# Kernel tuning notes

Measured on AMD Instinct MI355X. Metric: run time of the kernel, lower is better.

Reference implementation:

```python
import jax, jax.numpy as jnp
import numpy as np
import math

B, S, HID = 1, 2048, 4096
NH, NKV, HD = 32, 8, 128
N_REP = NH // NKV
ROPE_THETA = 10000.0


def setup_inputs() -> dict:
    key = jax.random.key(0)
    ks = jax.random.split(key, 5)
    hidden_states = jax.random.normal(ks[0], (B, S, HID), dtype=jnp.float32)
    # additive causal mask: 0 on/below diagonal, -1e9 above
    causal = jnp.triu(jnp.full((S, S), -1e9, dtype=jnp.float32), k=1)
    attention_mask = causal[None, None, :, :]
    wq = jax.random.normal(ks[1], (HID, NH * HD), dtype=jnp.float32) * 0.02
    wk = jax.random.normal(ks[2], (HID, NKV * HD), dtype=jnp.float32) * 0.02
    wv = jax.random.normal(ks[3], (HID, NKV * HD), dtype=jnp.float32) * 0.02
    wo = jax.random.normal(ks[4], (NH * HD, HID), dtype=jnp.float32) * 0.02
    return {"hidden_states": hidden_states, "attention_mask": attention_mask,
            "wq": wq, "wk": wk, "wv": wv, "wo": wo}


def _rope_cos_sin(seq_len, head_dim, base, dtype):
    inv_freq = 1.0 / (base ** (jnp.arange(0, head_dim, 2, dtype=jnp.float32) / head_dim))
    t = jnp.arange(seq_len, dtype=jnp.float32)
    freqs = jnp.outer(t, inv_freq)          # [S, HD/2]
    emb = jnp.concatenate([freqs, freqs], axis=-1)  # [S, HD]
    return jnp.cos(emb).astype(dtype), jnp.sin(emb).astype(dtype)


def _rotate_interleaved(x):
    # pairs (x0,x1) -> (-x1, x0), interleaved (matches torch stack/reshape trick)
    xp = x.reshape(*x.shape[:-1], -1, 2)
    return jnp.stack([-xp[..., 1], xp[..., 0]], axis=-1).reshape(x.shape)


def reference(hidden_states, attention_mask, wq, wk, wv, wo):
    b, s, _ = hidden_states.shape
    q = (hidden_states @ wq).reshape(b, s, NH, HD).transpose(0, 2, 1, 3)   # [B,NH,S,HD]
    k = (hidden_states @ wk).reshape(b, s, NKV, HD).transpose(0, 2, 1, 3)  # [B,NKV,S,HD]
    v = (hidden_states @ wv).reshape(b, s, NKV, HD).transpose(0, 2, 1, 3)

    cos, sin = _rope_cos_sin(s, HD, ROPE_THETA, hidden_states.dtype)
    cos = cos[None, None, :, :]  # broadcast over batch and heads
    sin = sin[None, None, :, :]
    q = q * cos + _rotate_interleaved(q) * sin
    k = k * cos + _rotate_interleaved(k) * sin

    # repeat_kv: [B,NKV,S,HD] -> [B,NH,S,HD]
    k = jnp.repeat(k, N_REP, axis=1)
    v = jnp.repeat(v, N_REP, axis=1)

    scores = jnp.einsum('bhqd,bhkd->bhqk', q, k) / math.sqrt(HD)
    scores = scores + attention_mask
    attn = jax.nn.softmax(scores.astype(jnp.float32), axis=-1).astype(q.dtype)
    out = jnp.einsum('bhqk,bhkd->bhqd', attn, v)          # [B,NH,S,HD]
    out = out.transpose(0, 2, 1, 3).reshape(b, s, NH * HD)
    return out @ wo
```

## Files before the change

kernel.cpp:

```cpp
#include <hip/hip_runtime.h>

#define S_LEN 2048
#define HID 4096
#define NH 32
#define NKV 8
#define HD 128
#define KVW 1024
#define NQKV 6144

typedef _Float16 f16;
typedef _Float16 f16x8 __attribute__((ext_vector_type(8)));
typedef _Float16 f16x4 __attribute__((ext_vector_type(4)));
typedef float f32x4 __attribute__((ext_vector_type(4)));
typedef float f32x16 __attribute__((ext_vector_type(16)));
typedef unsigned int u32;
typedef u32 u32x4 __attribute__((ext_vector_type(4)));

__device__ __forceinline__ void gll16(const void* g, void* lds) {
  __builtin_amdgcn_global_load_lds((const __attribute__((address_space(1))) void*)g,
                                   (__attribute__((address_space(3))) void*)lds, 16, 0, 0);
}

__global__ void k_cast(const float* __restrict__ src, f16* __restrict__ dst) {
  size_t i = ((size_t)blockIdx.x * blockDim.x + threadIdx.x) * 8;
  float4 a = *(const float4*)(src + i);
  float4 b = *(const float4*)(src + i + 4);
  f16x8 o = { (f16)a.x, (f16)a.y, (f16)a.z, (f16)a.w,
              (f16)b.x, (f16)b.y, (f16)b.z, (f16)b.w };
  *(f16x8*)(dst + i) = o;
}

__global__ void k_trig(float4* __restrict__ trig) {
  int id = blockIdx.x * blockDim.x + threadIdx.x;
  int s = id >> 6, i = id & 63;
  int j0 = 2 * i, j1 = 2 * i + 1;
  float f0 = powf(10000.f, -(float)(j0 & 63) / 64.f);
  float f1 = powf(10000.f, -(float)(j1 & 63) / 64.f);
  float a0 = (float)s * f0, a1 = (float)s * f1;
  trig[id] = make_float4(cosf(a0), cosf(a1), sinf(a0), sinf(a1));
}

__global__ void k_transpose(const float* __restrict__ src, f16* __restrict__ dst, int N) {
  __shared__ f16 tile[64][72];
  int nb = blockIdx.x * 64, kb = blockIdx.y * 64;
  int t = threadIdx.x;
  int kl = t >> 4, nc = (t & 15) << 2;
#pragma unroll
  for (int p = 0; p < 4; ++p) {
    int kk = kl + p * 16;
    float4 v = *(const float4*)(src + (size_t)(kb + kk) * N + nb + nc);
    f16x4 h = { (f16)v.x, (f16)v.y, (f16)v.z, (f16)v.w };
    *(f16x4*)(&tile[kk][nc]) = h;
  }
  __syncthreads();
  int nl = t >> 3, c = t & 7;
#pragma unroll
  for (int p = 0; p < 2; ++p) {
    int nn = nl + p * 32;
    f16x8 o;
#pragma unroll
    for (int i = 0; i < 8; ++i) o[i] = tile[c * 8 + i][nn];
    *(f16x8*)(dst + (size_t)(nb + nn) * HID + kb + c * 8) = o;
  }
}

#define SLOT 32768
extern __shared__ char smem[];

template<int MODE, int BNW, int SPLITK>
__global__ __launch_bounds__(512, 2) void k_gemm2(
    const f16* __restrict__ A, const f16* __restrict__ Bt, int K,
    f16* __restrict__ Qr, f16* __restrict__ Kr, f16* __restrict__ Vt,
    const float4* __restrict__ trig, float* __restrict__ Cout)
{
  constexpr int BN = BNW * 4;
  constexpr int NF = BNW / 16;
  const int tid = threadIdx.x, ln = tid & 63, w = tid >> 6;
  const int la = ln & 15, lg = ln >> 4;
  const int wr = w >> 2, wc = w & 3;
  const int m0 = blockIdx.y * 256, n0 = blockIdx.x * BN;
  const int Ksub = K / SPLITK;
  const int NKT = Ksub / 32;
  const int koff = (SPLITK > 1) ? blockIdx.z * Ksub : 0;
  float* Cp = (SPLITK > 1) ? Cout + (size_t)blockIdx.z * (size_t)S_LEN * HID : Cout;

  const char* gsrc[4];
  int ldst[4];
#pragma unroll
  for (int j = 0; j < 4; ++j) {
    int c = w * 4 + j;
    int rr = 16 * (c & 15) + (ln >> 2);
    int kq = ln & 3;
    size_t off;
    if (c < 16) {
      off = ((size_t)(m0 + rr) * K + koff + kq * 8) * 2;
      gsrc[j] = (const char*)A + off;
    } else {
      int br = (rr >= BN) ? rr - BN : rr;
      off = ((size_t)(n0 + br) * K + koff + kq * 8) * 2;
      gsrc[j] = (const char*)Bt + off;
    }
    ldst[j] = c * 1024;
  }

  f32x4 acc[8][NF] = {};

#pragma unroll
  for (int j = 0; j < 4; ++j) gll16(gsrc[j], smem + 0 * SLOT + ldst[j]);
#pragma unroll
  for (int j = 0; j < 4; ++j) gll16(gsrc[j] + 64, smem + 1 * SLOT + ldst[j]);
  asm volatile("s_waitcnt vmcnt(4)" ::: "memory");
  __builtin_amdgcn_s_barrier();

  for (int t = 0; t < NKT; ++t) {
    if (t + 2 < NKT) {
      char* sb = smem + ((t + 2) & 3) * SLOT;
#pragma unroll
      for (int j = 0; j < 4; ++j)
        gll16(gsrc[j] + (size_t)(t + 2) * 64, sb + ldst[j]);
    }
    const char* sb = smem + (t & 3) * SLOT;
    f16x8 af[8], bf[NF];
#pragma unroll
    for (int i = 0; i < 8; ++i)
      af[i] = *(const f16x8*)(sb + (wr * 128 + i * 16 + la) * 64 + lg * 16);
#pragma unroll
    for (int n = 0; n < NF; ++n)
      bf[n] = *(const f16x8*)(sb + 16384 + (wc * BNW + n * 16 + la) * 64 + lg * 16);
    __builtin_amdgcn_s_setprio(1);
#pragma unroll
    for (int i = 0; i < 8; ++i)
#pragma unroll
      for (int n = 0; n < NF; ++n)
        acc[i][n] = __builtin_amdgcn_mfma_f32_16x16x32_f16(af[i], bf[n], acc[i][n], 0, 0, 0);
    __builtin_amdgcn_s_setprio(0);
    if (t + 2 < NKT) asm volatile("s_waitcnt vmcnt(4)" ::: "memory");
    else             asm volatile("s_waitcnt vmcnt(0)" ::: "memory");
    __builtin_amdgcn_s_barrier();
  }

#pragma unroll
  for (int mi = 0; mi < 8; ++mi) {
#pragma unroll
    for (int nf = 0; nf < NF; ++nf) {
      f32x4 fr = acc[mi][nf];
      int n = n0 + wc * BNW + nf * 16 + la;
      int mr = m0 + wr * 128 + mi * 16 + lg * 4;
      if (MODE == 0) {
        if (n < HID + KVW) {
          int d = n & 127;
#pragma unroll
          for (int r = 0; r < 4; ++r) {
            float v = fr[r];
            float p = __shfl_xor(v, 1);
            float4 tc = trig[(size_t)(mr + r) * 64 + (d >> 1)];
            float cv = (d & 1) ? tc.y : tc.x;
            float sv = (d & 1) ? tc.w : tc.z;
            float o = v * cv + ((d & 1) ? p : -p) * sv;
            if (n < HID) Qr[(size_t)(mr + r) * HID + n] = (f16)o;
            else         Kr[(size_t)(mr + r) * KVW + (n - HID)] = (f16)o;
          }
        } else {
          int nv = n - (HID + KVW);
          f16x4 o4 = { (f16)fr[0], (f16)fr[1], (f16)fr[2], (f16)fr[3] };
          *(f16x4*)(Vt + (size_t)nv * S_LEN + mr) = o4;
        }
      } else {
#pragma unroll
        for (int r = 0; r < 4; ++r)
          Cp[(size_t)(mr + r) * HID + n] = fr[r];
      }
    }
  }
}

__global__ void k_reduce(const float* __restrict__ p0, const float* __restrict__ p1,
                         float* __restrict__ out) {
  size_t i = ((size_t)blockIdx.x * 256 + threadIdx.x) * 4;
  float4 a = *(const float4*)(p0 + i);
  float4 b = *(const float4*)(p1 + i);
  float4 o = make_float4(a.x + b.x, a.y + b.y, a.z + b.z, a.w + b.w);
  *(float4*)(out + i) = o;
}

#define KBYTES (64 * 128 * 2)
#define VBYTES (128 * 64 * 2)

__global__ __launch_bounds__(256, 2) void k_attn(
    const f16* __restrict__ Qr, const f16* __restrict__ Kr, const f16* __restrict__ Vt,
    f16* __restrict__ AO)
{
  int bid = blockIdx.x;
  int h, c;
  if (bid < 256) { h = bid >> 3; c = bid & 7; }
  else           { int t = bid - 256; h = t >> 3; c = 15 - (t & 7); }
  const int hkv = h >> 2;
  const int q0c = c * 128;
  const int NT = 2 * c + 2;

  __shared__ char KV[2][KBYTES + VBYTES];

  const int tid = threadIdx.x;
  const int ln = tid & 63, w = tid >> 6;
  const int q = ln & 31;
  const int hi = ln >> 5;
  const int qg = q0c + w * 32 + q;

  size_t ksrc[4], vsrc[4];
  int kdo[4], vdo[4];
#pragma unroll
  for (int j = 0; j < 4; ++j) {
    int kc = w * 4 + j;
    int kr = kc * 4 + (ln >> 4);
    ksrc[j] = ((size_t)kr * KVW + hkv * HD) * 2 + (size_t)(((ln & 15) ^ (kr & 7)) * 16);
    kdo[j] = kc * 1024;
    int vc = w * 4 + j;
    int d = vc * 8 + (ln >> 3);
    vsrc[j] = ((size_t)(hkv * HD + d) * S_LEN) * 2 + (size_t)(((ln & 7) ^ (d & 7)) * 16);
    vdo[j] = KBYTES + vc * 1024;
  }

  f16x8 qf[8];
  {
    const f16* qrow = Qr + (size_t)qg * HID + h * HD + hi * 8;
#pragma unroll
    for (int ks = 0; ks < 8; ++ks) qf[ks] = *(const f16x8*)(qrow + ks * 16);
  }

  f32x16 ot[4] = {};
  float m2 = -3.0e38f, l = 0.f;
  const float K2 = 0.12753256471f;

  int buf = 0;
#pragma unroll
  for (int j = 0; j < 4; ++j) {
    gll16((const char*)Kr + ksrc[j], &KV[0][kdo[j]]);
    gll16((const char*)Vt + vsrc[j], &KV[0][vdo[j]]);
  }

  for (int jt = 0; jt < NT; ++jt) {
    __syncthreads();
    if (jt + 1 < NT) {
      size_t ko = (size_t)(jt + 1) * 64 * KVW * 2;
      size_t vo = (size_t)(jt + 1) * 64 * 2;
#pragma unroll
      for (int j = 0; j < 4; ++j) {
        gll16((const char*)Kr + ksrc[j] + ko, &KV[buf ^ 1][kdo[j]]);
        gll16((const char*)Vt + vsrc[j] + vo, &KV[buf ^ 1][vdo[j]]);
      }
    }
    const int j0 = jt * 64;
    if (j0 <= q0c + w * 32 + 31) {
      const f16* Kb = (const f16*)&KV[buf][0];
      const f16* Vb = (const f16*)&KV[buf][KBYTES];
      f32x16 s0 = {}, s1 = {};
#pragma unroll
      for (int ks = 0; ks < 8; ++ks) {
        int cc = ((ks * 2 + hi) ^ (q & 7)) * 8;
        f16x8 k0 = *(const f16x8*)(Kb + q * 128 + cc);
        f16x8 k1 = *(const f16x8*)(Kb + (q + 32) * 128 + cc);
        s0 = __builtin_amdgcn_mfma_f32_32x32x16_f16(k0, qf[ks], s0, 0, 0, 0);
        s1 = __builtin_amdgcn_mfma_f32_32x32x16_f16(k1, qf[ks], s1, 0, 0, 0);
      }
      const bool nm = (j0 + 63 > q0c + w * 32);
      float p0[16], p1[16];
      float mx = -3.0e38f;
#pragma unroll
      for (int r = 0; r < 16; ++r) {
        float a = s0[r], b = s1[r];
        if (nm) {
          int kvb = j0 + (r & 3) + 8 * (r >> 2) + 4 * hi;
          if (kvb > qg) a = -3.0e38f;
          if (kvb + 32 > qg) b = -3.0e38f;
        }
        p0[r] = a; p1[r] = b;
        mx = fmaxf(mx, fmaxf(a, b));
      }
      mx = fmaxf(mx, __shfl_xor(mx, 32));
      float m2c = mx * K2;
      int defer = (m2c <= m2 + 11.0f);
      if (!__all(defer)) {
        float m2n = fmaxf(m2, m2c);
        float corr = exp2f(m2 - m2n);
        m2 = m2n; l *= corr;
#pragma unroll
        for (int t = 0; t < 4; ++t)
#pragma unroll
          for (int r = 0; r < 16; ++r) ot[t][r] *= corr;
      }
      float sum = 0.f;
#pragma unroll
      for (int r = 0; r < 16; ++r) {
        p0[r] = exp2f(__builtin_fmaf(p0[r], K2, -m2));
        p1[r] = exp2f(__builtin_fmaf(p1[r], K2, -m2));
        sum += p0[r] + p1[r];
      }
      l += sum + __shfl_xor(sum, 32);
      u32 pw0[8], pw1[8];
#pragma unroll
      for (int t = 0; t < 8; ++t) {
        pw0[t] = __builtin_bit_cast(u32, __builtin_amdgcn_cvt_pkrtz(p0[2 * t], p0[2 * t + 1]));
        pw1[t] = __builtin_bit_cast(u32, __builtin_amdgcn_cvt_pkrtz(p1[2 * t], p1[2 * t + 1]));
      }
      f16x8 pf[4];
#pragma unroll
      for (int ch = 0; ch < 2; ++ch) {
        const u32* pw = ch ? pw1 : pw0;
        u32 sx[8];
#pragma unroll
        for (int t = 0; t < 8; ++t) sx[t] = (u32)__shfl_xor((int)pw[t], 32);
        u32x4 fa = { hi ? sx[2] : pw[0], hi ? sx[3] : pw[1],
                     hi ? pw[2] : sx[0], hi ? pw[3] : sx[1] };
        u32x4 fb = { hi ? sx[6] : pw[4], hi ? sx[7] : pw[5],
                     hi ? pw[6] : sx[4], hi ? pw[7] : sx[5] };
        pf[ch * 2 + 0] = __builtin_bit_cast(f16x8, fa);
        pf[ch * 2 + 1] = __builtin_bit_cast(f16x8, fb);
      }
#pragma unroll
      for (int dt = 0; dt < 4; ++dt) {
        int d = dt * 32 + q;
#pragma unroll
        for (int f = 0; f < 4; ++f) {
          f16x8 vf = *(const f16x8*)(Vb + d * 64 + (((f * 2 + hi) ^ (q & 7)) * 8));
          ot[dt] = __builtin_amdgcn_mfma_f32_32x32x16_f16(vf, pf[f], ot[dt], 0, 0, 0);
        }
      }
    }
    buf ^= 1;
  }

  __syncthreads();
  char* scr = &KV[0][0] + w * 8192;
  float inv = 1.f / l;
#pragma unroll
  for (int dt = 0; dt < 4; ++dt) {
#pragma unroll
    for (int rg = 0; rg < 4; ++rg) {
      u32 wa = __builtin_bit_cast(u32, __builtin_amdgcn_cvt_pkrtz(ot[dt][rg * 4 + 0] * inv, ot[dt][rg * 4 + 1] * inv));
      u32 wb = __builtin_bit_cast(u32, __builtin_amdgcn_cvt_pkrtz(ot[dt][rg * 4 + 2] * inv, ot[dt][rg * 4 + 3] * inv));
      int byte = q * 256 + (((dt * 4 + rg) ^ (q & 7)) * 16) + hi * 8;
      u32* p = (u32*)(scr + byte);
      p[0] = wa; p[1] = wb;
    }
  }
  asm volatile("s_waitcnt lgkmcnt(0)" ::: "memory");
#pragma unroll
  for (int ps = 0; ps < 8; ++ps) {
    int qr = ps * 4 + (ln >> 4);
    int ck = (ln & 15) ^ (qr & 7);
    f16x8 v = *(const f16x8*)(scr + qr * 256 + ck * 16);
    *(f16x8*)(AO + (size_t)(q0c + w * 32 + qr) * HID + h * HD + (ln & 15) * 8) = v;
  }
}

extern "C" void kernel_launch(void* const* d_in, const int* in_sizes, int n_in,
                              void* d_out, int out_size, void* d_ws, size_t ws_size,
                              hipStream_t stream) {
  const float* hs = (const float*)d_in[0];
  const float* wq = (const float*)d_in[2];
  const float* wk = (const float*)d_in[3];
  const float* wv = (const float*)d_in[4];
  const float* wo = (const float*)d_in[5];
  float* out = (float*)d_out;

  char* ws = (char*)d_ws;
  size_t off = 0;
  auto alloc = [&](size_t b) { char* p = ws + off; off += (b + 255) & ~(size_t)255; return p; };
  f16* Hh   = (f16*)alloc((size_t)S_LEN * HID * 2);
  f16* Wt   = (f16*)alloc((size_t)NQKV * HID * 2);
  float4* trig = (float4*)alloc((size_t)S_LEN * 64 * sizeof(float4));
  f16* Qrp  = (f16*)alloc((size_t)S_LEN * HID * 2);
  f16* Krp  = (f16*)alloc((size_t)S_LEN * KVW * 2);
  f16* Vtp  = (f16*)alloc((size_t)KVW * S_LEN * 2);
  f16* AO   = (f16*)alloc((size_t)S_LEN * HID * 2);
  f16* Wot  = (f16*)alloc((size_t)HID * HID * 2);
  float* Pk = (float*)ws;

  hipFuncSetAttribute((const void*)k_gemm2<0, 48, 1>,
                      hipFuncAttributeMaxDynamicSharedMemorySize, 131072);
  hipFuncSetAttribute((const void*)k_gemm2<1, 64, 2>,
                      hipFuncAttributeMaxDynamicSharedMemorySize, 131072);

  k_cast<<<(S_LEN * HID) / (256 * 8), 256, 0, stream>>>(hs, Hh);
  k_trig<<<(S_LEN * 64) / 256, 256, 0, stream>>>(trig);
  k_transpose<<<dim3(HID / 64, HID / 64), 256, 0, stream>>>(wq, Wt, HID);
  k_transpose<<<dim3(KVW / 64, HID / 64), 256, 0, stream>>>(wk, Wt + (size_t)HID * HID, KVW);
  k_transpose<<<dim3(KVW / 64, HID / 64), 256, 0, stream>>>(wv, Wt + (size_t)(HID + KVW) * HID, KVW);
  k_transpose<<<dim3(HID / 64, HID / 64), 256, 0, stream>>>(wo, Wot, HID);
  k_gemm2<0, 48, 1><<<dim3(NQKV / 192, S_LEN / 256, 1), 512, 131072, stream>>>(
      Hh, Wt, HID, Qrp, Krp, Vtp, trig, nullptr);
  k_attn<<<dim3(512), 256, 0, stream>>>(Qrp, Krp, Vtp, AO);
  k_gemm2<1, 64, 2><<<dim3(HID / 256, S_LEN / 256, 2), 512, 131072, stream>>>(
      AO, Wot, HID, nullptr, nullptr, nullptr, nullptr, Pk);
  k_reduce<<<(S_LEN * HID) / (256 * 4), 256, 0, stream>>>(
      Pk, Pk + (size_t)S_LEN * HID, out);
}
```

Baseline: 368.1 us.

## Rewrite GEMM with 64-wide K tiles, XOR swizzle, and fine-grained staged pipeline

Replaces the GEMM kernel with one that loads 64-element K tiles into LDS using an XOR swizzle, so the fragment reads avoid bank conflicts. Each K step is split into four MFMA phases, with the A and B loads staged separately and interleaved between barriers. The output projection drops split-K and its reduce kernel in favor of a narrower 128-column tile, which removes the partial-sum buffer traffic. The cost is many more barriers per iteration and a different occupancy and tile balance.

Measured after the change: 337.6 us. 1.09x faster.

```diff
diff --git a/kernel.cpp b/kernel.cpp
--- a/kernel.cpp
+++ b/kernel.cpp
@@ -20,6 +20,7 @@
   __builtin_amdgcn_global_load_lds((const __attribute__((address_space(1))) void*)g,
                                    (__attribute__((address_space(3))) void*)lds, 16, 0, 0);
 }
+#define SFENCE asm volatile("" ::: "memory")
 
 __global__ void k_cast(const float* __restrict__ src, f16* __restrict__ dst) {
   size_t i = ((size_t)blockIdx.x * blockDim.x + threadIdx.x) * 8;
@@ -64,78 +65,127 @@
   }
 }
 
-#define SLOT 32768
 extern __shared__ char smem[];
 
-template<int MODE, int BNW, int SPLITK>
-__global__ __launch_bounds__(512, 2) void k_gemm2(
-    const f16* __restrict__ A, const f16* __restrict__ Bt, int K,
+template<int MODE, int BNW>
+__global__ __launch_bounds__(512, 2) void k_gemm3(
+    const f16* __restrict__ A, const f16* __restrict__ Bt,
     f16* __restrict__ Qr, f16* __restrict__ Kr, f16* __restrict__ Vt,
     const float4* __restrict__ trig, float* __restrict__ Cout)
 {
   constexpr int BN = BNW * 4;
   constexpr int NF = BNW / 16;
+  constexpr int BGLD = BN / 64;
+  constexpr int BSLOT = BN * 128;
+  constexpr int NT = 64;
   const int tid = threadIdx.x, ln = tid & 63, w = tid >> 6;
   const int la = ln & 15, lg = ln >> 4;
   const int wr = w >> 2, wc = w & 3;
   const int m0 = blockIdx.y * 256, n0 = blockIdx.x * BN;
-  const int Ksub = K / SPLITK;
-  const int NKT = Ksub / 32;
-  const int koff = (SPLITK > 1) ? blockIdx.z * Ksub : 0;
-  float* Cp = (SPLITK > 1) ? Cout + (size_t)blockIdx.z * (size_t)S_LEN * HID : Cout;
-
-  const char* gsrc[4];
-  int ldst[4];
-#pragma unroll
-  for (int j = 0; j < 4; ++j) {
-    int c = w * 4 + j;
-    int rr = 16 * (c & 15) + (ln >> 2);
-    int kq = ln & 3;
-    size_t off;
-    if (c < 16) {
-      off = ((size_t)(m0 + rr) * K + koff + kq * 8) * 2;
-      gsrc[j] = (const char*)A + off;
-    } else {
-      int br = (rr >= BN) ? rr - BN : rr;
-      off = ((size_t)(n0 + br) * K + koff + kq * 8) * 2;
-      gsrc[j] = (const char*)Bt + off;
-    }
-    ldst[j] = c * 1024;
-  }
+
+  const char* AsrcH[2][2];
+#pragma unroll
+  for (int h = 0; h < 2; ++h)
+#pragma unroll
+    for (int g = 0; g < 2; ++g) {
+      int r = h * 128 + g * 64 + w * 8 + (ln >> 3);
+      AsrcH[h][g] = (const char*)A +
+        ((size_t)(m0 + r) * HID + (size_t)(((ln & 7) ^ (r & 7)) * 8)) * 2;
+    }
+  const char* Bsrc[BGLD];
+#pragma unroll
+  for (int g = 0; g < BGLD; ++g) {
+    int r = g * 64 + w * 8 + (ln >> 3);
+    Bsrc[g] = (const char*)Bt +
+      ((size_t)(n0 + r) * HID + (size_t)(((ln & 7) ^ (r & 7)) * 8)) * 2;
+  }
+
+  auto stageA = [&](int t, int h) {
+    char* base = smem + (size_t)(((2 * t + h) & 3) * 16384) + w * 1024;
+    gll16(AsrcH[h][0] + (size_t)t * 128, base);
+    gll16(AsrcH[h][1] + (size_t)t * 128, base + 8192);
+  };
+  auto stageB = [&](int t) {
+    char* base = smem + 65536 + (size_t)((t & 1) * BSLOT) + w * 1024;
+#pragma unroll
+    for (int g = 0; g < BGLD; ++g)
+      gll16(Bsrc[g] + (size_t)t * 128, base + g * 8192);
+  };
+  auto ldA = [&](f16x8* dst, int t, int mh, int ks) {
+    const char* sb = smem + (size_t)(((2 * t + wr) & 3) * 16384);
+#pragma unroll
+    for (int i = 0; i < 4; ++i) {
+      int rl = (mh * 4 + i) * 16 + la;
+      dst[i] = *(const f16x8*)(sb + rl * 128 + (((ks * 4 + lg) ^ (rl & 7)) * 16));
+    }
+  };
+  auto ldB = [&](f16x8* dst, int t, int ks) {
+    const char* sb = smem + 65536 + (size_t)((t & 1) * BSLOT);
+#pragma unroll
+    for (int n = 0; n < NF; ++n) {
+      int r = wc * BNW + n * 16 + la;
+      dst[n] = *(const f16x8*)(sb + r * 128 + (((ks * 4 + lg) ^ (r & 7)) * 16));
+    }
+  };
 
   f32x4 acc[8][NF] = {};
-
-#pragma unroll
-  for (int j = 0; j < 4; ++j) gll16(gsrc[j], smem + 0 * SLOT + ldst[j]);
-#pragma unroll
-  for (int j = 0; j < 4; ++j) gll16(gsrc[j] + 64, smem + 1 * SLOT + ldst[j]);
-  asm volatile("s_waitcnt vmcnt(4)" ::: "memory");
+  f16x8 a0[4], a1[4], b0[NF], b1[NF];
+
+  stageA(0, 0); stageA(0, 1); stageB(0); stageB(1);
+  if constexpr (BGLD == 3) asm volatile("s_waitcnt vmcnt(3)" ::: "memory");
+  else                     asm volatile("s_waitcnt vmcnt(2)" ::: "memory");
   __builtin_amdgcn_s_barrier();
 
-  for (int t = 0; t < NKT; ++t) {
-    if (t + 2 < NKT) {
-      char* sb = smem + ((t + 2) & 3) * SLOT;
-#pragma unroll
-      for (int j = 0; j < 4; ++j)
-        gll16(gsrc[j] + (size_t)(t + 2) * 64, sb + ldst[j]);
-    }
-    const char* sb = smem + (t & 3) * SLOT;
-    f16x8 af[8], bf[NF];
-#pragma unroll
-    for (int i = 0; i < 8; ++i)
-      af[i] = *(const f16x8*)(sb + (wr * 128 + i * 16 + la) * 64 + lg * 16);
-#pragma unroll
-    for (int n = 0; n < NF; ++n)
-      bf[n] = *(const f16x8*)(sb + 16384 + (wc * BNW + n * 16 + la) * 64 + lg * 16);
+  for (int t = 0; t < NT; ++t) {
+    if (t + 1 < NT) stageA(t + 1, 0);
+    ldA(a0, t, 0, 0); ldB(b0, t, 0);
+    SFENCE; __builtin_amdgcn_s_barrier();
     __builtin_amdgcn_s_setprio(1);
 #pragma unroll
-    for (int i = 0; i < 8; ++i)
+    for (int i = 0; i < 4; ++i)
 #pragma unroll
       for (int n = 0; n < NF; ++n)
-        acc[i][n] = __builtin_amdgcn_mfma_f32_16x16x32_f16(af[i], bf[n], acc[i][n], 0, 0, 0);
+        acc[i][n] = __builtin_amdgcn_mfma_f32_16x16x32_f16(a0[i], b0[n], acc[i][n], 0, 0, 0);
     __builtin_amdgcn_s_setprio(0);
-    if (t + 2 < NKT) asm volatile("s_waitcnt vmcnt(4)" ::: "memory");
-    else             asm volatile("s_waitcnt vmcnt(0)" ::: "memory");
+    SFENCE; __builtin_amdgcn_s_barrier();
+    if (t + 1 < NT) stageA(t + 1, 1);
+    ldA(a1, t, 1, 0);
+    SFENCE; __builtin_amdgcn_s_barrier();
+    __builtin_amdgcn_s_setprio(1);
+#pragma unroll
+    for (int i = 0; i < 4; ++i)
+#pragma unroll
+      for (int n = 0; n < NF; ++n)
+        acc[4 + i][n] = __builtin_amdgcn_mfma_f32_16x16x32_f16(a1[i], b0[n], acc[4 + i][n], 0, 0, 0);
+    __builtin_amdgcn_s_setprio(0);
+    SFENCE; __builtin_amdgcn_s_barrier();
+    ldA(a0, t, 0, 1); ldB(b1, t, 1);
+    SFENCE; __builtin_amdgcn_s_barrier();
+    __builtin_amdgcn_s_setprio(1);
+#pragma unroll
+    for (int i = 0; i < 4; ++i)
+#pragma unroll
+      for (int n = 0; n < NF; ++n)
+        acc[i][n] = __builtin_amdgcn_mfma_f32_16x16x32_f16(a0[i], b1[n], acc[i][n], 0, 0, 0);
+    __builtin_amdgcn_s_setprio(0);
+    SFENCE; __builtin_amdgcn_s_barrier();
+    if (t + 2 < NT) stageB(t + 2);
+    ldA(a1, t, 1, 1);
+    SFENCE; __builtin_amdgcn_s_barrier();
+    __builtin_amdgcn_s_setprio(1);
+#pragma unroll
+    for (int i = 0; i < 4; ++i)
+#pragma unroll
+      for (int n = 0; n < NF; ++n)
+        acc[4 + i][n] = __builtin_amdgcn_mfma_f32_16x16x32_f16(a1[i], b1[n], acc[4 + i][n], 0, 0, 0);
+    __builtin_amdgcn_s_setprio(0);
+    SFENCE;
+    if (t < NT - 2) {
+      if constexpr (BGLD == 3) asm volatile("s_waitcnt vmcnt(3)" ::: "memory");
+      else                     asm volatile("s_waitcnt vmcnt(2)" ::: "memory");
+    } else if (t == NT - 2) {
+      asm volatile("s_waitcnt vmcnt(0)" ::: "memory");
+    }
     __builtin_amdgcn_s_barrier();
   }
 
@@ -168,19 +218,10 @@
       } else {
 #pragma unroll
         for (int r = 0; r < 4; ++r)
-          Cp[(size_t)(mr + r) * HID + n] = fr[r];
-      }
-    }
-  }
-}
-
-__global__ void k_reduce(const float* __restrict__ p0, const float* __restrict__ p1,
-                         float* __restrict__ out) {
-  size_t i = ((size_t)blockIdx.x * 256 + threadIdx.x) * 4;
-  float4 a = *(const float4*)(p0 + i);
-  float4 b = *(const float4*)(p1 + i);
-  float4 o = make_float4(a.x + b.x, a.y + b.y, a.z + b.z, a.w + b.w);
-  *(float4*)(out + i) = o;
+          Cout[(size_t)(mr + r) * HID + n] = fr[r];
+      }
+    }
+  }
 }
 
 #define KBYTES (64 * 128 * 2)
@@ -374,11 +415,10 @@
   f16* Vtp  = (f16*)alloc((size_t)KVW * S_LEN * 2);
   f16* AO   = (f16*)alloc((size_t)S_LEN * HID * 2);
   f16* Wot  = (f16*)alloc((size_t)HID * HID * 2);
-  float* Pk = (float*)ws;
-
-  hipFuncSetAttribute((const void*)k_gemm2<0, 48, 1>,
+
+  hipFuncSetAttribute((const void*)k_gemm3<0, 48>,
                       hipFuncAttributeMaxDynamicSharedMemorySize, 131072);
-  hipFuncSetAttribute((const void*)k_gemm2<1, 64, 2>,
+  hipFuncSetAttribute((const void*)k_gemm3<1, 32>,
                       hipFuncAttributeMaxDynamicSharedMemorySize, 131072);
 
   k_cast<<<(S_LEN * HID) / (256 * 8), 256, 0, stream>>>(hs, Hh);
@@ -387,11 +427,9 @@
   k_transpose<<<dim3(KVW / 64, HID / 64), 256, 0, stream>>>(wk, Wt + (size_t)HID * HID, KVW);
   k_transpose<<<dim3(KVW / 64, HID / 64), 256, 0, stream>>>(wv, Wt + (size_t)(HID + KVW) * HID, KVW);
   k_transpose<<<dim3(HID / 64, HID / 64), 256, 0, stream>>>(wo, Wot, HID);
-  k_gemm2<0, 48, 1><<<dim3(NQKV / 192, S_LEN / 256, 1), 512, 131072, stream>>>(
-      Hh, Wt, HID, Qrp, Krp, Vtp, trig, nullptr);
+  k_gemm3<0, 48><<<dim3(NQKV / 192, S_LEN / 256), 512, 114688, stream>>>(
+      Hh, Wt, Qrp, Krp, Vtp, trig, nullptr);
   k_attn<<<dim3(512), 256, 0, stream>>>(Qrp, Krp, Vtp, AO);
-  k_gemm2<1, 64, 2><<<dim3(HID / 256, S_LEN / 256, 2), 512, 131072, stream>>>(
-      AO, Wot, HID, nullptr, nullptr, nullptr, nullptr, Pk);
-  k_reduce<<<(S_LEN * HID) / (256 * 4), 256, 0, stream>>>(
-      Pk, Pk + (size_t)S_LEN * HID, out);
-}
+  k_gemm3<1, 32><<<dim3(HID / 128, S_LEN / 256), 512, 98304, stream>>>(
+      AO, Wot, nullptr, nullptr, nullptr, nullptr, out);
+}
```
